# Performance work log

Hardware: AMD Instinct MI355X
Metric: run time of the kernel (lower is better)

The kernel has to match this reference:

```python
import jax, jax.numpy as jnp
import numpy as np

N_NODES = 100000
N_EDGES = 400000
N_GRAPHS = 4096
D = 300          # emb_dim
L = 5            # num_layers
NUM_ATOM, NUM_CHIR = 120, 3
NUM_BOND, NUM_DIR = 6, 3
SELF_LOOP_BOND = 4
TEMP = 0.04


def setup_inputs() -> dict:
    key = jax.random.key(0)
    ks = jax.random.split(key, 24)
    inp = {}
    # graph batch 0
    inp["x0"] = jax.random.randint(ks[0], (N_NODES, 2), 0, 3)
    inp["edge_index0"] = jax.random.randint(ks[1], (2, N_EDGES), 0, N_NODES)
    inp["edge_attr0"] = jax.random.randint(ks[2], (N_EDGES, 2), 0, 3)
    inp["batch_ids0"] = jnp.sort(jax.random.randint(ks[3], (N_NODES,), 0, N_GRAPHS))
    inp["dangling0"] = jax.random.randint(ks[4], (N_GRAPHS,), 0, N_NODES)
    # graph batch 1
    inp["x1"] = jax.random.randint(ks[5], (N_NODES, 2), 0, 3)
    inp["edge_index1"] = jax.random.randint(ks[6], (2, N_EDGES), 0, N_NODES)
    inp["edge_attr1"] = jax.random.randint(ks[7], (N_EDGES, 2), 0, 3)
    inp["batch_ids1"] = jnp.sort(jax.random.randint(ks[8], (N_NODES,), 0, N_GRAPHS))
    inp["dangling1"] = jax.random.randint(ks[9], (N_GRAPHS,), 0, N_NODES)
    # shared encoder parameters
    g = lambda i, shp, s=0.1: (jax.random.normal(ks[i], shp, jnp.float32) * s)
    inp["atom_emb1"] = g(10, (NUM_ATOM, D))
    inp["atom_emb2"] = g(11, (NUM_CHIR, D))
    inp["eemb1"] = g(12, (L, NUM_BOND, D))
    inp["eemb2"] = g(13, (L, NUM_DIR, D))
    inp["W1"] = g(14, (L, D, 2 * D))
    inp["b1"] = jnp.zeros((L, 2 * D), jnp.float32)
    inp["W2"] = g(15, (L, 2 * D, D))
    inp["b2"] = jnp.zeros((L, D), jnp.float32)
    inp["bn_g"] = jnp.ones((L, D), jnp.float32)
    inp["bn_b"] = jnp.zeros((L, D), jnp.float32)
    # projectors stacked: 0=projector0, 1=projector1, 2=dangling_proj0, 3=dangling_proj1
    inp["pW1"] = g(16, (4, D, D))
    inp["pb1"] = jnp.zeros((4, D), jnp.float32)
    inp["pW2"] = g(17, (4, D, D))
    inp["pb2"] = jnp.zeros((4, D), jnp.float32)
    return inp


def _encode(x, edge_index, edge_attr, atom_emb1, atom_emb2,
            eemb1, eemb2, W1, b1, W2, b2, bn_g, bn_b):
    # initial node embedding: sum of atom-type and chirality embeddings
    h = atom_emb1[x[:, 0]] + atom_emb2[x[:, 1]]          # [N, D]
    src, dst = edge_index[0], edge_index[1]
    for l in range(L):
        e = eemb1[l][edge_attr[:, 0]] + eemb2[l][edge_attr[:, 1]]  # [E, D]
        msg = h[src] + e                                           # [E, D]
        agg = jax.ops.segment_sum(msg, dst, num_segments=h.shape[0])
        # self-loop with bond type 4, direction 0 (pretrain-gnns GINConv)
        agg = agg + h + eemb1[l][SELF_LOOP_BOND] + eemb2[l][0]
        z = jax.nn.relu(agg @ W1[l] + b1[l]) @ W2[l] + b2[l]       # GIN MLP
        mu = jnp.mean(z, axis=0)
        var = jnp.var(z, axis=0)
        z = (z - mu) * jax.lax.rsqrt(var + 1e-5) * bn_g[l] + bn_b[l]
        h = z if l == L - 1 else jax.nn.relu(z)                    # no ReLU on last layer
    return h


def _mlp(x, w1, bb1, w2, bb2):
    return jax.nn.relu(x @ w1 + bb1) @ w2 + bb2


def _branch(h, batch_ids, dangling, proj_i, dproj_i, pW1, pb1, pW2, pb2):
    pooled = jax.ops.segment_sum(h, batch_ids, num_segments=N_GRAPHS)
    counts = jax.ops.segment_sum(jnp.ones((h.shape[0],), h.dtype), batch_ids,
                                 num_segments=N_GRAPHS)
    pooled = pooled / jnp.maximum(counts, 1.0)[:, None]            # global_mean_pool
    out = _mlp(pooled, pW1[proj_i], pb1[proj_i], pW2[proj_i], pb2[proj_i])
    out = out + _mlp(h[dangling], pW1[dproj_i], pb1[dproj_i], pW2[dproj_i], pb2[dproj_i])
    return out / jnp.linalg.norm(out, axis=1, keepdims=True)       # L2 normalize


def reference(x0, edge_index0, edge_attr0, batch_ids0, dangling0,
              x1, edge_index1, edge_attr1, batch_ids1, dangling1,
              atom_emb1, atom_emb2, eemb1, eemb2, W1, b1, W2, b2, bn_g, bn_b,
              pW1, pb1, pW2, pb2):
    h0 = _encode(x0, edge_index0, edge_attr0, atom_emb1, atom_emb2,
                 eemb1, eemb2, W1, b1, W2, b2, bn_g, bn_b)
    f0 = _branch(h0, batch_ids0, dangling0, 0, 2, pW1, pb1, pW2, pb2)
    h1 = _encode(x1, edge_index1, edge_attr1, atom_emb1, atom_emb2,
                 eemb1, eemb2, W1, b1, W2, b2, bn_g, bn_b)
    f1 = _branch(h1, batch_ids1, dangling1, 1, 3, pW1, pb1, pW2, pb2)
    logits = (f0 @ f1.T) / TEMP                                    # [G, G]
    return logits
```

## Files before the change

### kernel.cpp

```cpp
#include <hip/hip_runtime.h>

#define NN    100000
#define NE    400000
#define NG    4096
#define LL    5
#define MPAD  100096
#define NCHUNK 98

typedef unsigned short u16;
typedef __attribute__((ext_vector_type(8))) _Float16 half8;
typedef __attribute__((ext_vector_type(4))) _Float16 hv4;
typedef __attribute__((ext_vector_type(4))) float float4v;
typedef __attribute__((ext_vector_type(16))) float float16v;
typedef __attribute__((ext_vector_type(8))) short short8v;

__device__ __forceinline__ float b2f(u16 u){
  union { float f; unsigned u; } c; c.u = ((unsigned)u)<<16; return c.f;
}
__device__ __forceinline__ u16 f2b(float f){
  union { float f; unsigned u; } c; c.f = f;
  unsigned x = c.u;
  return (u16)((x + 0x7fffu + ((x>>16)&1u)) >> 16);
}
__device__ __forceinline__ float h2f(u16 u){
  union { u16 s; _Float16 h; } c; c.s = u; return (float)c.h;
}
__device__ __forceinline__ u16 f2h(float f){
  union { u16 s; _Float16 h; } c; c.h = (_Float16)f; return c.s;
}
__device__ __forceinline__ void g2l16(const u16* g, u16* l){
  __builtin_amdgcn_global_load_lds((const __attribute__((address_space(1))) void*)g,
                                   (__attribute__((address_space(3))) void*)l, 16, 0, 0);
}

__global__ __launch_bounds__(256) void detect_dtype(const u16* __restrict__ p, int* __restrict__ flag){
  int i = blockIdx.x*256 + threadIdx.x;
  float v = b2f(p[i]);
  if (!(fabsf(v) <= 1e4f)) atomicOr(flag, 1);
}
__global__ __launch_bounds__(256) void cvt_param(const void* __restrict__ src, u16* __restrict__ dst,
                                                 int n, const int* __restrict__ flag){
  int i = blockIdx.x*256 + threadIdx.x;
  if (i >= n) return;
  float v = (*flag) ? ((const float*)src)[i] : b2f(((const u16*)src)[i]);
  dst[i] = f2h(v);
}

__global__ __launch_bounds__(256) void zero32(unsigned* __restrict__ p, int n){
  int i = blockIdx.x*256 + threadIdx.x;
  if (i < n) p[i] = 0u;
}

__global__ __launch_bounds__(256) void tpad(const u16* __restrict__ src, u16* __restrict__ dst,
                                            int L, int K, int N, int Kp, int Np){
  int idx = blockIdx.x*256 + threadIdx.x;
  if (idx >= L*Np*Kp) return;
  int l = idx/(Np*Kp); int r = idx - l*Np*Kp; int n = r/Kp; int k = r - n*Kp;
  dst[idx] = (n<N && k<K) ? src[(l*K + k)*N + n] : (u16)0;
}

__global__ __launch_bounds__(256) void ecomb_build(const u16* __restrict__ ee1, const u16* __restrict__ ee2,
                                                   u16* __restrict__ ec){
  int idx = blockIdx.x*256 + threadIdx.x;
  if (idx >= LL*18*160) return;
  int l = idx/(18*160); int r = idx - l*18*160; int c = r/160; int p = r - c*160;
  int a0 = c/3, a1 = c - a0*3;
  u16 o0=0,o1=0;
  if (p < 150){
    int d = 2*p;
    o0 = f2h(h2f(ee1[(l*6+a0)*300+d  ]) + h2f(ee2[(l*3+a1)*300+d  ]));
    o1 = f2h(h2f(ee1[(l*6+a0)*300+d+1]) + h2f(ee2[(l*3+a1)*300+d+1]));
  }
  ((ushort2*)ec)[idx] = make_ushort2(o0,o1);
}

__global__ __launch_bounds__(256) void node_init(const int* __restrict__ x, const u16* __restrict__ ae1,
                                                 const u16* __restrict__ ae2, u16* __restrict__ h){
  int idx = blockIdx.x*256 + threadIdx.x;
  if (idx >= MPAD*160) return;
  int n = idx/160, p = idx - n*160;
  u16 o0=0,o1=0;
  if (n < NN && p < 150){
    int a = x[2*n], ch = x[2*n+1];
    int d = 2*p;
    o0 = f2h(h2f(ae1[a*300+d  ]) + h2f(ae2[ch*300+d  ]));
    o1 = f2h(h2f(ae1[a*300+d+1]) + h2f(ae2[ch*300+d+1]));
  }
  ((ushort2*)h)[idx] = make_ushort2(o0,o1);
}

__global__ __launch_bounds__(256) void hist(const int* __restrict__ ei, int* __restrict__ counts){
  int e = blockIdx.x*256 + threadIdx.x;
  if (e >= NE) return;
  atomicAdd(&counts[ei[NE + e]], 1);
}
__global__ __launch_bounds__(256) void scan_chunks(const int* __restrict__ counts, int* __restrict__ csums){
  __shared__ int sd[256];
  int base = blockIdx.x*1024;
  int s = 0;
  for (int i = threadIdx.x; i < 1024; i += 256){ int g = base+i; if (g < NN) s += counts[g]; }
  sd[threadIdx.x] = s; __syncthreads();
  for (int off=128; off>0; off>>=1){ if (threadIdx.x < off) sd[threadIdx.x] += sd[threadIdx.x+off]; __syncthreads(); }
  if (threadIdx.x == 0) csums[blockIdx.x] = sd[0];
}
__global__ __launch_bounds__(128) void scan_base(const int* __restrict__ csums, int* __restrict__ cbase,
                                                 int* __restrict__ offsets){
  __shared__ int sd[128];
  int tid = threadIdx.x;
  int v = (tid < NCHUNK) ? csums[tid] : 0;
  sd[tid] = v; __syncthreads();
  for (int off=1; off<128; off<<=1){
    int t = (tid >= off) ? sd[tid-off] : 0; __syncthreads();
    sd[tid] += t; __syncthreads();
  }
  if (tid < NCHUNK) cbase[tid] = sd[tid] - v;
  if (tid == 0) offsets[NN] = sd[NCHUNK-1];
}
__global__ __launch_bounds__(256) void scan_final(const int* __restrict__ counts, const int* __restrict__ cbase,
                                                  int* __restrict__ offsets){
  __shared__ int sd[256];
  int tid = threadIdx.x;
  int base = blockIdx.x*1024 + tid*4;
  int v0 = (base   < NN) ? counts[base  ] : 0;
  int v1 = (base+1 < NN) ? counts[base+1] : 0;
  int v2 = (base+2 < NN) ? counts[base+2] : 0;
  int v3 = (base+3 < NN) ? counts[base+3] : 0;
  int s = v0+v1+v2+v3;
  sd[tid] = s; __syncthreads();
  for (int off=1; off<256; off<<=1){
    int t = (tid >= off) ? sd[tid-off] : 0; __syncthreads();
    sd[tid] += t; __syncthreads();
  }
  int run = cbase[blockIdx.x] + sd[tid] - s;
  if (base   < NN){ offsets[base  ] = run; } run += v0;
  if (base+1 < NN){ offsets[base+1] = run; } run += v1;
  if (base+2 < NN){ offsets[base+2] = run; } run += v2;
  if (base+3 < NN){ offsets[base+3] = run; }
}
__global__ __launch_bounds__(256) void fill_perm(const int* __restrict__ ei, const int* __restrict__ ea,
                                                 const int* __restrict__ offsets,
                                                 int* __restrict__ cursor, int* __restrict__ pk){
  int e = blockIdx.x*256 + threadIdx.x;
  if (e >= NE) return;
  int d = ei[NE + e];
  int src = ei[e];
  int c = ea[2*e]*3 + ea[2*e+1];
  int pos = offsets[d] + atomicAdd(&cursor[d], 1);
  pk[pos] = src*32 + c;
}

__global__ __launch_bounds__(256) void aggregate(
    const u16* __restrict__ h, const u16* __restrict__ ecL,
    const int* __restrict__ offsets, const int* __restrict__ pk,
    u16* __restrict__ agg,
    const float* __restrict__ sc, const float* __restrict__ sh, int dobn)
{
  __shared__ u16 ecs[18*320];
  for (int i = threadIdx.x; i < 18*160; i += 256)
    ((ushort2*)ecs)[i] = ((const ushort2*)ecL)[i];
  __syncthreads();
  int node = blockIdx.x*4 + (threadIdx.x>>6);
  int lane = threadIdx.x & 63;
  bool tl = lane < 16;
  hv4 s0 = (hv4)(_Float16)1, t0 = (hv4)(_Float16)0;
  hv4 s1 = (hv4)(_Float16)1, t1 = (hv4)(_Float16)0;
  if (dobn){
    #pragma unroll
    for (int j=0;j<4;++j){ s0[j] = (_Float16)sc[lane*4+j]; t0[j] = (_Float16)sh[lane*4+j]; }
    if (tl){
      #pragma unroll
      for (int j=0;j<4;++j){ s1[j] = (_Float16)sc[256+lane*4+j]; t1[j] = (_Float16)sh[256+lane*4+j]; }
    }
  }
  const hv4 hz = (hv4)(_Float16)0;
  auto bn0 = [&](hv4 v)->hv4 {
    if (!dobn) return v;
    return __builtin_elementwise_max(v*s0 + t0, hz);
  };
  auto bn1 = [&](hv4 v)->hv4 {
    if (!dobn) return v;
    return __builtin_elementwise_max(v*s1 + t1, hz);
  };
  const hv4* h4 = (const hv4*)h;
  const hv4* e4 = (const hv4*)ecs;
  long base = (long)node*80;
  hv4 acc0, acc1 = hz;
  acc0 = bn0(h4[base + lane]) + e4[12*80 + lane];
  if (tl) acc1 = bn1(h4[base + 64 + lane]) + e4[12*80 + 64 + lane];
  if (node < NN){
    int s = offsets[node], en = offsets[node+1];
    int i = s;
    while (i + 3 < en){
      int p0 = pk[i], p1 = pk[i+1], p2 = pk[i+2], p3 = pk[i+3]; i += 4;
      long b0 = (long)(p0>>5)*80, b1 = (long)(p1>>5)*80;
      long b2 = (long)(p2>>5)*80, b3 = (long)(p3>>5)*80;
      int c0 = (p0&31)*80, c1 = (p1&31)*80, c2 = (p2&31)*80, c3 = (p3&31)*80;
      hv4 a0 = bn0(h4[b0+lane]), a1 = bn0(h4[b1+lane]);
      hv4 a2 = bn0(h4[b2+lane]), a3 = bn0(h4[b3+lane]);
      hv4 e0 = e4[c0+lane], e1 = e4[c1+lane], e2 = e4[c2+lane], e3 = e4[c3+lane];
      acc0 += (a0+e0); acc0 += (a1+e1); acc0 += (a2+e2); acc0 += (a3+e3);
      if (tl){
        hv4 x0 = bn1(h4[b0+64+lane]), x1 = bn1(h4[b1+64+lane]);
        hv4 x2 = bn1(h4[b2+64+lane]), x3 = bn1(h4[b3+64+lane]);
        hv4 y0 = e4[c0+64+lane], y1 = e4[c1+64+lane];
        hv4 y2 = e4[c2+64+lane], y3 = e4[c3+64+lane];
        acc1 += (x0+y0); acc1 += (x1+y1); acc1 += (x2+y2); acc1 += (x3+y3);
      }
    }
    while (i < en){
      int p0 = pk[i]; ++i;
      long b0 = (long)(p0>>5)*80; int c0 = (p0&31)*80;
      acc0 += (bn0(h4[b0+lane]) + e4[c0+lane]);
      if (tl) acc1 += (bn1(h4[b0+64+lane]) + e4[c0+64+lane]);
    }
  }
  hv4* a4 = (hv4*)agg;
  __builtin_nontemporal_store(acc0, &a4[base + lane]);
  if (tl) __builtin_nontemporal_store(acc1, &a4[base + 64 + lane]);
}

__global__ __launch_bounds__(512, 2) void gin_mlp(
    const u16* __restrict__ A,
    const u16* __restrict__ W1Tl,
    const u16* __restrict__ b1l,
    const u16* __restrict__ W2Tl,
    const u16* __restrict__ b2l,
    u16* __restrict__ Z,
    float* __restrict__ colsum, float* __restrict__ colsumsq)
{
  __shared__ __align__(16) u16 lds[32768];
  u16* uS = lds;
  u16* Ws = lds + 8192;
  int tid = threadIdx.x;
  int wave = tid>>6, lane = tid&63;
  int n5 = lane & 31, hi = lane >> 5;
  int q = lane>>4, r = lane&15;
  int rg = wave>>1, ch = wave&1;
  int wr = wave>>2, wc = wave&3;
  int m0 = blockIdx.x*128;

  half8 aReg[20];
  const u16* Arow = A + (long)(m0 + rg*32 + n5)*320 + hi*8;
  #pragma unroll
  for (int kc=0; kc<20; ++kc) aReg[kc] = *(const half8*)(Arow + kc*16);

  float4v zacc[4][6];
  #pragma unroll
  for (int i=0;i<4;i++)
    #pragma unroll
    for (int j=0;j<6;j++) zacc[i][j] = (float4v){0.f,0.f,0.f,0.f};

  for (int t1=0; t1<10; ++t1){
    int n1_0 = t1*64;
    __syncthreads();
    #pragma unroll
    for (int rnd=0; rnd<5; ++rnd){
      int ck = rnd*512 + tid;
      int n = ck/41, k8 = ck - n*41;
      const u16* src = (k8 < 40) ? (W1Tl + (long)(n1_0 + n)*320 + k8*8) : W1Tl;
      g2l16(src, Ws + ck*8);
    }
    if (tid < 64){
      int ck = 2560 + tid;
      int n = ck/41, k8 = ck - n*41;
      const u16* src = (k8 < 40) ? (W1Tl + (long)(n1_0 + n)*320 + k8*8) : W1Tl;
      g2l16(src, Ws + ck*8);
    }
    __syncthreads();
    float16v uacc = (float16v)(0.f);
    #pragma unroll
    for (int kc=0; kc<20; ++kc){
      half8 bw = *(const half8*)&Ws[(ch*32 + n5)*328 + kc*16 + hi*8];
      uacc = __builtin_amdgcn_mfma_f32_32x32x16_f16(aReg[kc], bw, uacc, 0,0,0);
    }
    {
      int n1g = n1_0 + ch*32 + n5;
      float bv = (n1g < 600) ? h2f(b1l[n1g]) : 0.f;
      u16* uw = uS + ch*4096 + n5;
      #pragma unroll
      for (int reg=0; reg<16; ++reg){
        int row = rg*32 + (reg&3) + 8*(reg>>2) + 4*hi;
        float v = fmaxf(uacc[reg] + bv, 0.f);
        uw[row*32] = f2h(v);
      }
    }
    __syncthreads();
    #pragma unroll
    for (int i=0;i<6;i++){
      int idx = tid*8 + i*4096;
      int kc2 = idx / 12288;
      int rem = idx - kc2*12288;
      int n2 = rem >> 5, k8 = rem & 31;
      g2l16(W2Tl + (long)n2*640 + n1_0 + kc2*32 + k8, Ws + idx);
    }
    __syncthreads();
    #pragma unroll
    for (int kc2=0; kc2<2; ++kc2){
      half8 af[4], bf[6];
      #pragma unroll
      for (int i=0;i<4;i++) af[i] = *(const half8*)&uS[kc2*4096 + (wr*64+i*16+r)*32 + q*8];
      #pragma unroll
      for (int j=0;j<6;j++) bf[j] = *(const half8*)&Ws[kc2*12288 + (wc*96+j*16+r)*32 + q*8];
      #pragma unroll
      for (int i=0;i<4;i++)
        #pragma unroll
        for (int j=0;j<6;j++)
          zacc[i][j] = __builtin_amdgcn_mfma_f32_16x16x32_f16(af[i], bf[j], zacc[i][j], 0,0,0);
    }
  }
  #pragma unroll
  for (int j=0;j<6;j++){
    int c = wc*96 + j*16 + r;
    float bv = (c < 300) ? h2f(b2l[c]) : 0.f;
    float s1 = 0.f, s2 = 0.f;
    #pragma unroll
    for (int i=0;i<4;i++){
      int rowb = m0 + wr*64 + i*16 + q*4;
      #pragma unroll
      for (int t=0;t<4;t++){
        float v = zacc[i][j][t] + bv;
        int gr = rowb + t;
        if (c < 320) Z[(long)gr*320 + c] = f2h(v);
        if (gr < NN){ s1 += v; s2 += v*v; }
      }
    }
    s1 += __shfl_xor(s1,16); s1 += __shfl_xor(s1,32);
    s2 += __shfl_xor(s2,16); s2 += __shfl_xor(s2,32);
    if (q == 0 && c < 384){ atomicAdd(&colsum[c], s1); atomicAdd(&colsumsq[c], s2); }
  }
}

__global__ __launch_bounds__(256) void gemm_nt(
    const u16* __restrict__ A, int lda,
    const u16* __restrict__ BT, int ldb,
    int Kp,
    const u16* __restrict__ bias, int Nreal,
    float scale, int dorelu, int omode, int Ncap,
    void* __restrict__ Cv, int ldc,
    const int* __restrict__ outmode)
{
  __shared__ __align__(16) u16 As[3][128*32];
  __shared__ __align__(16) u16 Bs[3][128*32];
  int tid = threadIdx.x;
  int wave = tid>>6, lane = tid&63;
  int wr = (wave>>1)&1, wc = wave&1;
  int nwg  = gridDim.x*gridDim.y;
  int flat = blockIdx.y*gridDim.x + blockIdx.x;
  int qd = nwg>>3, rm = nwg&7;
  int xcd = flat&7, sub = flat>>3;
  int wgid = (xcd<rm ? xcd*(qd+1) : rm*(qd+1)+(xcd-rm)*qd) + sub;
  int nt = wgid % gridDim.x, mt = wgid / gridDim.x;
  int m0 = mt*128, n0 = nt*128;
  int q = lane>>4, r = lane&15;
  int srow = tid>>2, scol = (tid&3)*8;
  const u16* Ag0 = A  + (long)(m0+srow)*lda + scol;
  const u16* Ag1 = A  + (long)(m0+64+srow)*lda + scol;
  const u16* Bg0 = BT + (long)(n0+srow)*ldb + scol;
  const u16* Bg1 = BT + (long)(n0+64+srow)*ldb + scol;
  float4v acc[4][4];
  #pragma unroll
  for (int i=0;i<4;i++)
    #pragma unroll
    for (int j=0;j<4;j++) acc[i][j] = (float4v){0.f,0.f,0.f,0.f};

  int nk = Kp >> 5;
  {
    g2l16(Ag0, &As[0][tid*8]);     g2l16(Ag1, &As[0][2048+tid*8]);
    g2l16(Bg0, &Bs[0][tid*8]);     g2l16(Bg1, &Bs[0][2048+tid*8]);
    if (nk > 1){
      g2l16(Ag0+32, &As[1][tid*8]);  g2l16(Ag1+32, &As[1][2048+tid*8]);
      g2l16(Bg0+32, &Bs[1][tid*8]);  g2l16(Bg1+32, &Bs[1][2048+tid*8]);
    }
  }
  for (int t=0; t<nk; ++t){
    int cur = t % 3;
    if (t+1 < nk) asm volatile("s_waitcnt vmcnt(4)" ::: "memory");
    else          asm volatile("s_waitcnt vmcnt(0)" ::: "memory");
    __builtin_amdgcn_s_barrier();
    if (t+2 < nk){
      int b = (t+2)%3, k0 = (t+2)*32;
      g2l16(Ag0+k0, &As[b][tid*8]);  g2l16(Ag1+k0, &As[b][2048+tid*8]);
      g2l16(Bg0+k0, &Bs[b][tid*8]);  g2l16(Bg1+k0, &Bs[b][2048+tid*8]);
    }
    half8 af[4], bf[4];
    #pragma unroll
    for (int i=0;i<4;i++) af[i] = *(const half8*)&As[cur][(wr*64+i*16+r)*32 + q*8];
    #pragma unroll
    for (int j=0;j<4;j++) bf[j] = *(const half8*)&Bs[cur][(wc*64+j*16+r)*32 + q*8];
    #pragma unroll
    for (int i=0;i<4;i++)
      #pragma unroll
      for (int j=0;j<4;j++)
        acc[i][j] = __builtin_amdgcn_mfma_f32_16x16x32_f16(af[i], bf[j], acc[i][j], 0,0,0);
  }

  int ob = omode;
  if (outmode) ob = (*outmode) ? 0 : 1;
  u16* Ch = (u16*)Cv; float* Cf = (float*)Cv;
  #pragma unroll
  for (int j=0;j<4;j++){
    int c = n0 + wc*64 + j*16 + r;
    float bv = (bias && c < Nreal) ? h2f(bias[c]) : 0.f;
    #pragma unroll
    for (int i=0;i<4;i++){
      int rowb = m0 + wr*64 + i*16 + q*4;
      #pragma unroll
      for (int tt=0; tt<4; ++tt){
        float v = acc[i][j][tt] + bv;
        if (dorelu) v = fmaxf(v, 0.f);
        v *= scale;
        int gr = rowb + tt;
        if (c < Ncap){
          long o = (long)gr*ldc + c;
          if (ob == 2)      Ch[o] = f2h(v);
          else if (ob == 1) Ch[o] = f2b(v);
          else              Cf[o] = v;
        }
      }
    }
  }
}

__global__ __launch_bounds__(320) void bn_finalize(const float* __restrict__ st, const u16* __restrict__ g,
                                                   const u16* __restrict__ b, float* __restrict__ sc,
                                                   float* __restrict__ sh){
  int c = threadIdx.x;
  if (c >= 300){ sc[c] = 0.f; sh[c] = 0.f; return; }
  float mu  = st[c] * (1.0f/NN);
  float var = st[384+c] * (1.0f/NN) - mu*mu;
  float inv = rsqrtf(var + 1e-5f);
  float gg = h2f(g[c]) * inv;
  sc[c] = gg; sh[c] = h2f(b[c]) - mu*gg;
}
__global__ __launch_bounds__(256) void bn_apply(const u16* __restrict__ z, const float* __restrict__ sc,
                                                const float* __restrict__ sh, u16* __restrict__ h, int dorelu){
  int idx = blockIdx.x*256 + threadIdx.x;
  if (idx >= NN*40) return;
  int n = idx/40, p = idx - n*40;
  short8v zz = ((const short8v*)z)[(long)n*40 + p];
  short8v out;
  #pragma unroll
  for (int e=0; e<8; ++e){
    int d = p*8 + e;
    float v = h2f((u16)zz[e])*sc[d] + sh[d];
    if (dorelu) v = fmaxf(v, 0.f);
    out[e] = (short)f2h(v);
    if (d >= 300) out[e] = 0;
  }
  ((short8v*)h)[(long)n*40 + p] = out;
}

__global__ __launch_bounds__(256) void graph_starts(const int* __restrict__ ids, int* __restrict__ starts){
  int i = blockIdx.x*256 + threadIdx.x;
  if (i >= NN) return;
  int b = ids[i];
  if (i == 0){ for (int g=0; g<=b; ++g) starts[g] = 0; }
  else { int p = ids[i-1]; for (int g=p+1; g<=b; ++g) starts[g] = i; }
  if (i == NN-1){ for (int g=b+1; g<=NG; ++g) starts[g] = NN; }
}
__global__ __launch_bounds__(256) void pool_kernel(const u16* __restrict__ h, const int* __restrict__ starts,
                                                   u16* __restrict__ pooled){
  int g = blockIdx.x*4 + (threadIdx.x>>6);
  int lane = threadIdx.x & 63;
  if (g >= NG) return;
  int s = starts[g], e = starts[g+1];
  int cnt = e - s; if (cnt < 1) cnt = 1;
  float inv = 1.0f/(float)cnt;
  float ax[3] = {0,0,0}, ay[3] = {0,0,0};
  const ushort2* h2 = (const ushort2*)h;
  for (int row=s; row<e; ++row){
    long base = (long)row*160;
    #pragma unroll
    for (int jp=0; jp<3; ++jp){
      int p = jp*64 + lane;
      if (p < 160){ ushort2 v = h2[base+p]; ax[jp] += h2f(v.x); ay[jp] += h2f(v.y); }
    }
  }
  ushort2* o2 = (ushort2*)pooled;
  #pragma unroll
  for (int jp=0; jp<3; ++jp){
    int p = jp*64 + lane;
    if (p < 160) o2[g*160+p] = make_ushort2(f2h(ax[jp]*inv), f2h(ay[jp]*inv));
  }
}
__global__ __launch_bounds__(256) void gather_rows(const u16* __restrict__ h, const int* __restrict__ idxs,
                                                   u16* __restrict__ out){
  int idx = blockIdx.x*256 + threadIdx.x;
  if (idx >= NG*160) return;
  int g = idx/160, p = idx - g*160;
  ((ushort2*)out)[idx] = ((const ushort2*)h)[(long)idxs[g]*160 + p];
}
__global__ __launch_bounds__(256) void add_norm(const float* __restrict__ vp, const float* __restrict__ vd,
                                                u16* __restrict__ f){
  int g = blockIdx.x*4 + (threadIdx.x>>6);
  int lane = threadIdx.x & 63;
  if (g >= NG) return;
  float vals[5]; float ss = 0.f;
  #pragma unroll
  for (int t=0; t<5; ++t){
    int d = lane + 64*t; float v = 0.f;
    if (d < 300) v = vp[g*320+d] + vd[g*320+d];
    vals[t] = v; ss += v*v;
  }
  #pragma unroll
  for (int off=32; off>0; off>>=1) ss += __shfl_xor(ss, off);
  float inv = rsqrtf(ss);
  #pragma unroll
  for (int t=0; t<5; ++t){
    int d = lane + 64*t;
    if (d < 320) f[g*320+d] = f2h(d < 300 ? vals[t]*inv : 0.f);
  }
}

extern "C" void kernel_launch(void* const* d_in, const int* in_sizes, int n_in,
                              void* d_out, int out_size, void* d_ws, size_t ws_size,
                              hipStream_t stream)
{
  const int* xin[2]  = {(const int*)d_in[0], (const int*)d_in[5]};
  const int* ei[2]   = {(const int*)d_in[1], (const int*)d_in[6]};
  const int* ea[2]   = {(const int*)d_in[2], (const int*)d_in[7]};
  const int* bid[2]  = {(const int*)d_in[3], (const int*)d_in[8]};
  const int* dang[2] = {(const int*)d_in[4], (const int*)d_in[9]};
  (void)in_sizes; (void)n_in; (void)out_size; (void)ws_size;

  char* w = (char*)d_ws;
  auto alloc = [&](size_t bytes)->char* {
    char* p = w; w += (bytes + 255) & ~(size_t)255; return p;
  };
  u16* Zb   = (u16*)alloc((size_t)MPAD*320*2);
  u16* Gb   = (u16*)alloc((size_t)MPAD*320*2);
  u16*   pooled = (u16*)alloc((size_t)NG*320*2);
  u16*   hd     = (u16*)alloc((size_t)NG*320*2);
  u16*   ubuf   = (u16*)alloc((size_t)NG*384*2);
  float* vpb    = (float*)alloc((size_t)NG*320*4);
  float* vdb    = (float*)alloc((size_t)NG*320*4);
  u16* ec   = (u16*)alloc((size_t)LL*18*320*2);
  u16* W1T  = (u16*)alloc((size_t)LL*640*320*2);
  u16* W2T  = (u16*)alloc((size_t)LL*384*640*2);
  u16* pW1T = (u16*)alloc((size_t)4*384*320*2);
  u16* pW2T = (u16*)alloc((size_t)4*384*384*2);
  int* counts = (int*)alloc((size_t)NN*4);
  int* cursor = (int*)alloc((size_t)NN*4);
  int* offs   = (int*)alloc((size_t)(NN+1)*4);
  int* perm   = (int*)alloc((size_t)NE*4);
  int* csums  = (int*)alloc(512);
  int* cbase  = (int*)alloc(512);
  float* stats = (float*)alloc(768*4);
  float* bnsc  = (float*)alloc(384*4);
  float* bnsh  = (float*)alloc(384*4);
  int* starts  = (int*)alloc((size_t)(NG+1)*4);
  u16* f0b     = (u16*)alloc((size_t)NG*320*2);
  u16* f1b     = (u16*)alloc((size_t)NG*320*2);
  int* dflag   = (int*)alloc(256);
  const int pcnt[14] = {36000, 900, 9000, 4500, 900000, 3000, 900000, 1500,
                        1500, 1500, 360000, 1200, 360000, 1200};
  u16* parena = (u16*)alloc((size_t)2580300*2 + 14*256);
  u16* pp[14];
  { size_t off = 0;
    for (int i=0;i<14;i++){ pp[i] = parena + off; off += (size_t)((pcnt[i]+127)&~127); } }
  u16* ae1 = pp[0];  u16* ae2 = pp[1];  u16* ee1 = pp[2];  u16* ee2 = pp[3];
  u16* W1  = pp[4];  u16* b1  = pp[5];  u16* W2  = pp[6];  u16* b2  = pp[7];
  u16* bng = pp[8];  u16* bnb = pp[9];  u16* pW1 = pp[10]; u16* pb1 = pp[11];
  u16* pW2 = pp[12]; u16* pb2 = pp[13];

  auto cdiv = [](long a, long b){ return (int)((a + b - 1)/b); };
  auto gemm = [&](const u16* A, int lda, const u16* BT, int ldb, int Kp,
                  const u16* bias, int Nreal, float scale, int relu, int omode, int Ncap,
                  void* C, int ldc, int gx, int gy, const int* om){
    gemm_nt<<<dim3(gx,gy), 256, 0, stream>>>(A,lda,BT,ldb,Kp,bias,Nreal,scale,relu,omode,Ncap,
                                             C,ldc,om);
  };

  zero32<<<1,256,0,stream>>>((unsigned*)dflag, 1);
  detect_dtype<<<16,256,0,stream>>>((const u16*)d_in[14], dflag);
  for (int i=0;i<14;i++)
    cvt_param<<<cdiv(pcnt[i],256),256,0,stream>>>(d_in[10+i], pp[i], pcnt[i], dflag);

  tpad<<<cdiv((long)LL*640*320,256),256,0,stream>>>(W1,  W1T,  LL, 300, 600, 320, 640);
  tpad<<<cdiv((long)LL*384*640,256),256,0,stream>>>(W2,  W2T,  LL, 600, 300, 640, 384);
  tpad<<<cdiv((long)4*384*320,256),256,0,stream>>>(pW1, pW1T, 4,  300, 300, 320, 384);
  tpad<<<cdiv((long)4*384*384,256),256,0,stream>>>(pW2, pW2T, 4,  300, 300, 384, 384);
  ecomb_build<<<cdiv((long)LL*18*160,256),256,0,stream>>>(ee1, ee2, ec);

  for (int br=0; br<2; ++br){
    u16* fo = br ? f1b : f0b;
    node_init<<<cdiv((long)MPAD*160,256),256,0,stream>>>(xin[br], ae1, ae2, Zb);
    zero32<<<cdiv(NN,256),256,0,stream>>>((unsigned*)counts, NN);
    hist<<<cdiv(NE,256),256,0,stream>>>(ei[br], counts);
    scan_chunks<<<NCHUNK,256,0,stream>>>(counts, csums);
    scan_base<<<1,128,0,stream>>>(csums, cbase, offs);
    scan_final<<<NCHUNK,256,0,stream>>>(counts, cbase, offs);
    zero32<<<cdiv(NN,256),256,0,stream>>>((unsigned*)cursor, NN);
    fill_perm<<<cdiv(NE,256),256,0,stream>>>(ei[br], ea[br], offs, cursor, perm);

    for (int l=0; l<LL; ++l){
      aggregate<<<MPAD/4,256,0,stream>>>(Zb, ec + (size_t)l*18*320, offs, perm, Gb,
                                         bnsc, bnsh, (l > 0) ? 1 : 0);
      zero32<<<3,256,0,stream>>>((unsigned*)stats, 768);
      gin_mlp<<<MPAD/128, 512, 0, stream>>>(Gb,
          W1T + (size_t)l*640*320, b1 + l*600,
          W2T + (size_t)l*384*640, b2 + l*300,
          Zb, stats, stats+384);
      bn_finalize<<<1,320,0,stream>>>(stats, bng + l*300, bnb + l*300, bnsc, bnsh);
    }
    bn_apply<<<cdiv((long)NN*40,256),256,0,stream>>>(Zb, bnsc, bnsh, Gb, 0);

    graph_starts<<<cdiv(NN,256),256,0,stream>>>(bid[br], starts);
    pool_kernel<<<NG/4,256,0,stream>>>(Gb, starts, pooled);
    gather_rows<<<cdiv((long)NG*160,256),256,0,stream>>>(Gb, dang[br], hd);

    int pi = br, dpi = 2 + br;
    gemm(pooled, 320, pW1T + (size_t)pi*384*320, 320, 320,
         pb1 + pi*300, 300, 1.f, 1, 2, 384, ubuf, 384, 3, NG/128, nullptr);
    gemm(ubuf, 384, pW2T + (size_t)pi*384*384, 384, 384,
         pb2 + pi*300, 300, 1.f, 0, 0, 320, vpb, 320, 3, NG/128, nullptr);
    gemm(hd, 320, pW1T + (size_t)dpi*384*320, 320, 320,
         pb1 + dpi*300, 300, 1.f, 1, 2, 384, ubuf, 384, 3, NG/128, nullptr);
    gemm(ubuf, 384, pW2T + (size_t)dpi*384*384, 384, 384,
         pb2 + dpi*300, 300, 1.f, 0, 0, 320, vdb, 320, 3, NG/128, nullptr);
    add_norm<<<NG/4,256,0,stream>>>(vpb, vdb, fo);
  }

  gemm(f0b, 320, f1b, 320, 320, nullptr, 0, 25.0f, 0, 1, NG,
       d_out, NG, NG/128, NG/128, dflag);
}
```

Measured before the change: 3.559 ms.

## Restructure GIN MLP kernel into 32-wide hidden chunks with co-loaded W1/W2 tiles

The fused two-layer MLP kernel now walks the hidden dimension in 32-column chunks instead of 64. It loads the W1 and W2 tiles together before a single barrier, which removes one __syncthreads per iteration. The first GEMM switches from 32x32x16 to 16x16x32 MFMA, and the intermediate tile in LDS uses an XOR swizzle to avoid bank conflicts. LDS use drops, but the number of iterations and barriers doubles.

```diff
diff --git a/kernel.cpp b/kernel.cpp
--- a/kernel.cpp
+++ b/kernel.cpp
@@ -11,7 +11,6 @@
 typedef __attribute__((ext_vector_type(8))) _Float16 half8;
 typedef __attribute__((ext_vector_type(4))) _Float16 hv4;
 typedef __attribute__((ext_vector_type(4))) float float4v;
-typedef __attribute__((ext_vector_type(16))) float float16v;
 typedef __attribute__((ext_vector_type(8))) short short8v;
 
 __device__ __forceinline__ float b2f(u16 u){
@@ -228,21 +227,27 @@
     u16* __restrict__ Z,
     float* __restrict__ colsum, float* __restrict__ colsumsq)
 {
-  __shared__ __align__(16) u16 lds[32768];
-  u16* uS = lds;
-  u16* Ws = lds + 8192;
+  __shared__ __align__(16) u16 lds[26880];
+  u16* uS  = lds;
+  u16* W1s = lds + 4096;
+  u16* W2s = lds + 4096 + 10496;
   int tid = threadIdx.x;
   int wave = tid>>6, lane = tid&63;
-  int n5 = lane & 31, hi = lane >> 5;
   int q = lane>>4, r = lane&15;
   int rg = wave>>1, ch = wave&1;
   int wr = wave>>2, wc = wave&3;
   int m0 = blockIdx.x*128;
 
-  half8 aReg[20];
-  const u16* Arow = A + (long)(m0 + rg*32 + n5)*320 + hi*8;
-  #pragma unroll
-  for (int kc=0; kc<20; ++kc) aReg[kc] = *(const half8*)(Arow + kc*16);
+  half8 aReg0[10], aReg1[10];
+  {
+    const u16* Arow0 = A + (long)(m0 + rg*32 + r)*320 + q*8;
+    const u16* Arow1 = A + (long)(m0 + rg*32 + 16 + r)*320 + q*8;
+    #pragma unroll
+    for (int kc=0; kc<10; ++kc){
+      aReg0[kc] = *(const half8*)(Arow0 + kc*32);
+      aReg1[kc] = *(const half8*)(Arow1 + kc*32);
+    }
+  }
 
   float4v zacc[4][6];
   #pragma unroll
@@ -250,64 +255,62 @@
     #pragma unroll
     for (int j=0;j<6;j++) zacc[i][j] = (float4v){0.f,0.f,0.f,0.f};
 
-  for (int t1=0; t1<10; ++t1){
-    int n1_0 = t1*64;
+  for (int t1=0; t1<20; ++t1){
+    int n1_0 = t1*32;
     __syncthreads();
     #pragma unroll
-    for (int rnd=0; rnd<5; ++rnd){
-      int ck = rnd*512 + tid;
-      int n = ck/41, k8 = ck - n*41;
-      const u16* src = (k8 < 40) ? (W1Tl + (long)(n1_0 + n)*320 + k8*8) : W1Tl;
-      g2l16(src, Ws + ck*8);
-    }
-    if (tid < 64){
-      int ck = 2560 + tid;
-      int n = ck/41, k8 = ck - n*41;
-      const u16* src = (k8 < 40) ? (W1Tl + (long)(n1_0 + n)*320 + k8*8) : W1Tl;
-      g2l16(src, Ws + ck*8);
+    for (int rnd=0; rnd<3; ++rnd){
+      int c = rnd*512 + tid;
+      if (c < 1312){
+        int n = c/41, k8 = c - n*41;
+        const u16* src = (k8 < 40) ? (W1Tl + (long)(n1_0 + n)*320 + k8*8) : W1Tl;
+        g2l16(src, W1s + c*8);
+      }
+    }
+    #pragma unroll
+    for (int rnd=0; rnd<3; ++rnd){
+      int i = rnd*512 + tid;
+      int n2 = i>>2, k8 = (i&3)*8;
+      g2l16(W2Tl + (long)n2*640 + n1_0 + k8, W2s + i*8);
     }
     __syncthreads();
-    float16v uacc = (float16v)(0.f);
-    #pragma unroll
-    for (int kc=0; kc<20; ++kc){
-      half8 bw = *(const half8*)&Ws[(ch*32 + n5)*328 + kc*16 + hi*8];
-      uacc = __builtin_amdgcn_mfma_f32_32x32x16_f16(aReg[kc], bw, uacc, 0,0,0);
+
+    float4v ua0 = (float4v){0.f,0.f,0.f,0.f}, ua1 = (float4v){0.f,0.f,0.f,0.f};
+    #pragma unroll
+    for (int kc=0; kc<10; ++kc){
+      half8 bw = *(const half8*)&W1s[(ch*16 + r)*328 + kc*32 + q*8];
+      ua0 = __builtin_amdgcn_mfma_f32_16x16x32_f16(aReg0[kc], bw, ua0, 0,0,0);
+      ua1 = __builtin_amdgcn_mfma_f32_16x16x32_f16(aReg1[kc], bw, ua1, 0,0,0);
     }
     {
-      int n1g = n1_0 + ch*32 + n5;
-      float bv = (n1g < 600) ? h2f(b1l[n1g]) : 0.f;
-      u16* uw = uS + ch*4096 + n5;
+      int col = ch*16 + r;
+      int n1c = n1_0 + col;
+      float bv = (n1c < 600) ? h2f(b1l[n1c]) : 0.f;
       #pragma unroll
-      for (int reg=0; reg<16; ++reg){
-        int row = rg*32 + (reg&3) + 8*(reg>>2) + 4*hi;
-        float v = fmaxf(uacc[reg] + bv, 0.f);
-        uw[row*32] = f2h(v);
+      for (int reg=0; reg<4; ++reg){
+        int row0 = rg*32 + q*4 + reg;
+        int row1 = row0 + 16;
+        uS[(row0*32 + col) ^ ((row0&7)<<3)] = f2h(fmaxf(ua0[reg] + bv, 0.f));
+        uS[(row1*32 + col) ^ ((row1&7)<<3)] = f2h(fmaxf(ua1[reg] + bv, 0.f));
       }
     }
     __syncthreads();
-    #pragma unroll
-    for (int i=0;i<6;i++){
-      int idx = tid*8 + i*4096;
-      int kc2 = idx / 12288;
-      int rem = idx - kc2*12288;
-      int n2 = rem >> 5, k8 = rem & 31;
-      g2l16(W2Tl + (long)n2*640 + n1_0 + kc2*32 + k8, Ws + idx);
-    }
-    __syncthreads();
-    #pragma unroll
-    for (int kc2=0; kc2<2; ++kc2){
-      half8 af[4], bf[6];
+
+    half8 af[4], bf[6];
+    #pragma unroll
+    for (int i=0;i<4;i++){
+      int row = wr*64 + i*16 + r;
+      af[i] = *(const half8*)&uS[(row*32 + q*8) ^ ((row&7)<<3)];
+    }
+    #pragma unroll
+    for (int j=0;j<6;j++) bf[j] = *(const half8*)&W2s[(wc*96 + j*16 + r)*32 + q*8];
+    #pragma unroll
+    for (int i=0;i<4;i++)
       #pragma unroll
-      for (int i=0;i<4;i++) af[i] = *(const half8*)&uS[kc2*4096 + (wr*64+i*16+r)*32 + q*8];
-      #pragma unroll
-      for (int j=0;j<6;j++) bf[j] = *(const half8*)&Ws[kc2*12288 + (wc*96+j*16+r)*32 + q*8];
-      #pragma unroll
-      for (int i=0;i<4;i++)
-        #pragma unroll
-        for (int j=0;j<6;j++)
-          zacc[i][j] = __builtin_amdgcn_mfma_f32_16x16x32_f16(af[i], bf[j], zacc[i][j], 0,0,0);
-    }
-  }
+      for (int j=0;j<6;j++)
+        zacc[i][j] = __builtin_amdgcn_mfma_f32_16x16x32_f16(af[i], bf[j], zacc[i][j], 0,0,0);
+  }
+
   #pragma unroll
   for (int j=0;j<6;j++){
     int c = wc*96 + j*16 + r;
```

New measurement: 3.777 ms. 1.06x slower.
